# Kernel optimization log

Measured on AMD Instinct MI355X. Metric: run time of the kernel, lower is better.

The kernel has to match this reference:

```python
import jax, jax.numpy as jnp
import numpy as np

NEG_INF = -1e10  # matches torch's -10000000000.0 fill


def setup_inputs() -> dict:
    key = jax.random.key(0)
    k1, k2, k3, k4, k5, k6 = jax.random.split(key, 6)
    B, N, D_IN, D_HID, D_OUT = 8, 2048, 512, 512, 512
    H = jax.random.normal(k1, (B, N, D_IN), dtype=jnp.float32)
    bias = jax.random.normal(k2, (B, N, N), dtype=jnp.float32)
    mask = jax.random.randint(k3, (B, N, N), 0, 2, dtype=jnp.int32)
    s = 1.0 / np.sqrt(D_IN)
    Wq = jax.random.normal(k4, (D_IN, D_HID), dtype=jnp.float32) * s
    Wk = jax.random.normal(k5, (D_IN, D_HID), dtype=jnp.float32) * s
    Wv = jax.random.normal(k6, (D_IN, D_OUT), dtype=jnp.float32) * s
    return {"H": H, "bias": bias, "mask": mask, "Wq": Wq, "Wk": Wk, "Wv": Wv}


def reference(H, bias, mask, Wq, Wk, Wv):
    # Q,K: [B,N,d_hid], V: [B,N,d_out]
    Q = H @ Wq
    K = H @ Wk
    V = H @ Wv
    d = Q.shape[-1]
    scale = 1.0 / jnp.sqrt(jnp.asarray(d, dtype=Q.dtype))
    # scores: [B,N,N]; scale, add bias, then fill masked-out entries
    scores = jnp.einsum("bnd,bmd->bnm", Q, K) * scale + bias
    scores = jnp.where(mask == 0, jnp.asarray(NEG_INF, scores.dtype), scores)
    atn = jax.nn.softmax(scores, axis=-1)
    return jnp.einsum("bnm,bmo->bno", atn, V)
```

## Files before the change

### kernel.cpp

```cpp
#include <hip/hip_runtime.h>
#include <hip/hip_bf16.h>

typedef __attribute__((ext_vector_type(8))) short short8;
typedef __attribute__((ext_vector_type(4))) float floatx4;
typedef __attribute__((ext_vector_type(4))) int intx4;
typedef __attribute__((ext_vector_type(4))) unsigned short ushortx4;

#define NB 8
#define NN 2048
#define DD 512

__device__ __forceinline__ unsigned short f2bf(float f) {
  union { float f; unsigned int u; } v; v.f = f;
  unsigned int u = v.u;
  return (unsigned short)((u + 0x7fffu + ((u >> 16) & 1u)) >> 16);
}
__device__ __forceinline__ float bf2f(unsigned short s) {
  union { unsigned int u; float f; } v; v.u = ((unsigned int)s) << 16;
  return v.f;
}

typedef __attribute__((address_space(3))) unsigned short lds_us;
typedef __attribute__((address_space(1))) const unsigned short glb_us;

__device__ __forceinline__ void ld_lds16(const unsigned short* g, unsigned short* l) {
  __builtin_amdgcn_global_load_lds((glb_us*)g, (lds_us*)l, 16, 0, 0);
}

__global__ __launch_bounds__(256) void mha_cvtH(const float* __restrict__ H,
                                                unsigned short* __restrict__ Hb, int n8) {
  int i = blockIdx.x * 256 + threadIdx.x;
  if (i >= n8) return;
  const float4* src = (const float4*)H;
  float4 a = src[2 * i], b = src[2 * i + 1];
  short8 o;
  o[0] = (short)f2bf(a.x); o[1] = (short)f2bf(a.y); o[2] = (short)f2bf(a.z); o[3] = (short)f2bf(a.w);
  o[4] = (short)f2bf(b.x); o[5] = (short)f2bf(b.y); o[6] = (short)f2bf(b.z); o[7] = (short)f2bf(b.w);
  *(short8*)(Hb + 8 * i) = o;
}

__global__ __launch_bounds__(256) void mha_prep(const floatx4* __restrict__ bias,
                                                const intx4* __restrict__ mask,
                                                ushortx4* __restrict__ bm) {
  int i = blockIdx.x * 256 + threadIdx.x;
  floatx4 bv = __builtin_nontemporal_load(&bias[i]);
  intx4 mv = __builtin_nontemporal_load(&mask[i]);
  const unsigned short NINF = 0xFF80;
  ushortx4 o;
  o.x = mv.x ? f2bf(bv.x) : NINF;
  o.y = mv.y ? f2bf(bv.y) : NINF;
  o.z = mv.z ? f2bf(bv.z) : NINF;
  o.w = mv.w ? f2bf(bv.w) : NINF;
  __builtin_nontemporal_store(o, &bm[i]);
}

__global__ __launch_bounds__(256) void mha_tW(const float* __restrict__ Wq, const float* __restrict__ Wk,
                                              const float* __restrict__ Wv,
                                              unsigned short* __restrict__ Wqt, unsigned short* __restrict__ Wkt,
                                              unsigned short* __restrict__ Wvt) {
  const float* W = (blockIdx.z == 0) ? Wq : (blockIdx.z == 1) ? Wk : Wv;
  unsigned short* Wt = (blockIdx.z == 0) ? Wqt : (blockIdx.z == 1) ? Wkt : Wvt;
  __shared__ float tile[32][33];
  int d0 = blockIdx.x * 32, k0 = blockIdx.y * 32;
  int t = threadIdx.x, r = t >> 3, c4 = (t & 7) * 4;
  float4 v = *(const float4*)(W + (size_t)(k0 + r) * DD + d0 + c4);
  tile[r][c4] = v.x; tile[r][c4 + 1] = v.y; tile[r][c4 + 2] = v.z; tile[r][c4 + 3] = v.w;
  __syncthreads();
  union { unsigned short s[4]; uint2 v; } u;
  u.s[0] = f2bf(tile[c4][r]);     u.s[1] = f2bf(tile[c4 + 1][r]);
  u.s[2] = f2bf(tile[c4 + 2][r]); u.s[3] = f2bf(tile[c4 + 3][r]);
  *(uint2*)(Wt + (size_t)(d0 + r) * DD + k0 + c4) = u.v;
}

__global__ __launch_bounds__(256) void mha_tV(const unsigned short* __restrict__ Vr,
                                              unsigned short* __restrict__ Vt) {
  int b = blockIdx.z;
  int d0 = blockIdx.x * 32, n0 = blockIdx.y * 32;
  __shared__ unsigned short tile[32][34];
  int t = threadIdx.x, r = t >> 3, c4 = (t & 7) * 4;
  union { uint2 v; unsigned short s[4]; } u;
  u.v = *(const uint2*)(Vr + ((size_t)b * NN + n0 + r) * DD + d0 + c4);
  tile[r][c4] = u.s[0]; tile[r][c4 + 1] = u.s[1]; tile[r][c4 + 2] = u.s[2]; tile[r][c4 + 3] = u.s[3];
  __syncthreads();
  union { unsigned short s[4]; uint2 v; } o;
  o.s[0] = tile[c4][r]; o.s[1] = tile[c4 + 1][r]; o.s[2] = tile[c4 + 2][r]; o.s[3] = tile[c4 + 3][r];
  *(uint2*)(Vt + ((size_t)b * DD + d0 + r) * NN + n0 + c4) = o.v;
}

__device__ __forceinline__ void stage_tile_async(const unsigned short* __restrict__ g, int ld,
                                                 unsigned short* s, int t) {
#pragma unroll
  for (int h = 0; h < 2; ++h) {
    int c = t + h * 256;
    int r = c >> 2, p = c & 3;
    int seg = (p - (r >> 1)) & 3;
    ld_lds16(g + (size_t)r * ld + seg * 8, s + c * 8);
  }
}

__device__ __forceinline__ void mfma_step(const unsigned short* As, const unsigned short* Bs,
                                          int wr, int wc, int quad, int lr, floatx4 acc[4][4]) {
  short8 a[4], b[4];
#pragma unroll
  for (int i = 0; i < 4; ++i) {
    int ra = wr * 64 + i * 16 + lr;
    int rb = wc * 64 + i * 16 + lr;
    a[i] = *(const short8*)(As + ra * 32 + ((quad + (ra >> 1)) & 3) * 8);
    b[i] = *(const short8*)(Bs + rb * 32 + ((quad + (rb >> 1)) & 3) * 8);
  }
  __builtin_amdgcn_s_setprio(1);
#pragma unroll
  for (int i = 0; i < 4; ++i)
#pragma unroll
    for (int j = 0; j < 4; ++j)
      acc[i][j] = __builtin_amdgcn_mfma_f32_16x16x32_bf16(a[i], b[j], acc[i][j], 0, 0, 0);
  __builtin_amdgcn_s_setprio(0);
}

__global__ __launch_bounds__(256) void mha_proj(const unsigned short* __restrict__ Hb,
                                                const unsigned short* __restrict__ Wqt,
                                                const unsigned short* __restrict__ Wkt,
                                                const unsigned short* __restrict__ Wvt,
                                                unsigned short* __restrict__ Qb,
                                                unsigned short* __restrict__ Kb,
                                                unsigned short* __restrict__ Vr) {
  const unsigned short* Wt = (blockIdx.z == 0) ? Wqt : (blockIdx.z == 1) ? Wkt : Wvt;
  unsigned short* dst = (blockIdx.z == 0) ? Qb : (blockIdx.z == 1) ? Kb : Vr;
  __shared__ unsigned short As[128 * 64], Bs[128 * 64];
  int t = threadIdx.x, wave = t >> 6, lane = t & 63, quad = lane >> 4, lr = lane & 15;
  int wr = wave >> 1, wc = wave & 1;
  int m0 = blockIdx.y * 128, n0 = blockIdx.x * 128;
  floatx4 acc[4][4] = {};
  for (int k0 = 0; k0 < DD; k0 += 64) {
    __syncthreads();
    stage_tile_async(Hb + (size_t)m0 * DD + k0, DD, As, t);
    stage_tile_async(Hb + (size_t)m0 * DD + k0 + 32, DD, As + 4096, t);
    stage_tile_async(Wt + (size_t)n0 * DD + k0, DD, Bs, t);
    stage_tile_async(Wt + (size_t)n0 * DD + k0 + 32, DD, Bs + 4096, t);
    __syncthreads();
    mfma_step(As, Bs, wr, wc, quad, lr, acc);
    mfma_step(As + 4096, Bs + 4096, wr, wc, quad, lr, acc);
  }
#pragma unroll
  for (int i = 0; i < 4; ++i)
#pragma unroll
    for (int j = 0; j < 4; ++j)
#pragma unroll
      for (int r = 0; r < 4; ++r) {
        int row = m0 + wr * 64 + i * 16 + quad * 4 + r;
        int col = n0 + wc * 64 + j * 16 + lr;
        dst[(size_t)row * DD + col] = f2bf(acc[i][j][r]);
      }
}


template <int SQ>
__device__ __forceinline__ void qk_stage(const unsigned short* Ks, const short8* q,
                                         int wj, int quad, int lr, floatx4 (&acc_s)[4]) {
  __builtin_amdgcn_s_setprio(1);
#pragma unroll
  for (int kc = 0; kc < 4; ++kc) {
#pragma unroll
    for (int jt = 0; jt < 4; ++jt) {
      int rb = wj * 64 + jt * 16 + lr;
      short8 bf = *(const short8*)(Ks + kc * 4096 + rb * 32 + ((quad + (rb >> 1)) & 3) * 8);
      acc_s[jt] = __builtin_amdgcn_mfma_f32_16x16x32_bf16(q[SQ * 4 + kc], bf, acc_s[jt], 0, 0, 0);
    }
  }
  __builtin_amdgcn_s_setprio(0);
}

template <int JC>
__device__ __forceinline__ void pv_stage(const unsigned short* Vs, const unsigned short* Ps,
                                         int wave, int quad, int lr, floatx4 (&acc_o)[4][4]) {
  short8 pa[4];
#pragma unroll
  for (int it = 0; it < 4; ++it)
    pa[it] = *(const short8*)(Ps + (it * 16 + lr) * 128 + ((JC * 32 + quad * 8) ^ ((lr & 7) << 3)));
  __builtin_amdgcn_s_setprio(1);
#pragma unroll
  for (int dt = 0; dt < 4; ++dt) {
    int rb = wave * 64 + dt * 16 + lr;
    short8 bf = *(const short8*)(Vs + rb * 32 + ((quad + (rb >> 1)) & 3) * 8);
#pragma unroll
    for (int it = 0; it < 4; ++it)
      acc_o[it][dt] = __builtin_amdgcn_mfma_f32_16x16x32_bf16(pa[it], bf, acc_o[it][dt], 0, 0, 0);
  }
  __builtin_amdgcn_s_setprio(0);
}

__global__ __launch_bounds__(512) void mha_attn(const unsigned short* __restrict__ Qb,
                                                const unsigned short* __restrict__ Kb,
                                                const unsigned short* __restrict__ Vtb,
                                                const unsigned short* __restrict__ bmE,
                                                float* __restrict__ out) {
  __shared__ unsigned short KV[2][16384];
  __shared__ unsigned short Ps[64 * 128];
  __shared__ unsigned short Bm[64 * 128];
  __shared__ float ls[64];

  const int b = blockIdx.x;
  const int i0 = blockIdx.y * 64;
  const int t = threadIdx.x;
  const int wave = t >> 6, lane = t & 63, quad = lane >> 4, lr = lane & 15;
  const int wi = wave & 3;
  const int wj = wave >> 2;
  const float scale = 0.04419417382415922f;

  const unsigned short* Q = Qb + (size_t)b * NN * DD;
  const unsigned short* K = Kb + (size_t)b * NN * DD;
  const unsigned short* V = Vtb + (size_t)b * DD * NN;
  const unsigned short* bm = bmE + (size_t)b * NN * NN;

  if (t < 64) ls[t] = 0.0f;

  short8 q[16];
#pragma unroll
  for (int kc = 0; kc < 16; ++kc)
    q[kc] = *(const short8*)(Q + (size_t)(i0 + wi * 16 + lr) * DD + kc * 32 + quad * 8);

  floatx4 acc_o[4][4] = {};
  float rs[4] = {0.f, 0.f, 0.f, 0.f};

  const int krow = t >> 2, kphys = t & 3;
  const int kseg = (kphys - (krow >> 1)) & 3;

#pragma unroll
  for (int h = 0; h < 4; ++h)
    ld_lds16(K + (size_t)krow * DD + h * 32 + kseg * 8, KV[0] + h * 4096 + t * 8);
#pragma unroll
  for (int h = 0; h < 2; ++h) {
    int c = t + h * 512, row = c >> 4, phys = c & 15, seg = (phys - row) & 15;
    ld_lds16(bm + (size_t)(i0 + row) * NN + seg * 8, Bm + c * 8);
  }
  __syncthreads();

  for (int tt = 0; tt < 16; ++tt) {
    const int j0 = tt * 128;
    floatx4 acc_s[4] = {};

#pragma unroll
    for (int s = 0; s < 4; ++s) {
      if (s < 3) {
#pragma unroll
        for (int h = 0; h < 4; ++h)
          ld_lds16(K + (size_t)(j0 + krow) * DD + (s + 1) * 128 + h * 32 + kseg * 8,
                   KV[(s + 1) & 1] + h * 4096 + t * 8);
      } else {
#pragma unroll
        for (int h = 0; h < 4; ++h) {
          int c = t + h * 512, row = c >> 2, phys = c & 3, seg = (phys - (row >> 1)) & 3;
          ld_lds16(V + (size_t)row * NN + j0 + seg * 8, KV[0] + c * 8);
        }
      }
      if (s == 0) qk_stage<0>(KV[0], q, wj, quad, lr, acc_s);
      if (s == 1) qk_stage<1>(KV[1], q, wj, quad, lr, acc_s);
      if (s == 2) qk_stage<2>(KV[0], q, wj, quad, lr, acc_s);
      if (s == 3) {
        qk_stage<3>(KV[1], q, wj, quad, lr, acc_s);
#pragma unroll
        for (int jt = 0; jt < 4; ++jt) {
          int col = wj * 64 + jt * 16 + lr;
#pragma unroll
          for (int rr = 0; rr < 4; ++rr) {
            int row = wi * 16 + quad * 4 + rr;
            float bi = bf2f(Bm[row * 128 + ((((col >> 3) + row) & 15) << 3) + (col & 7)]);
            float e = __expf(acc_s[jt][rr] * scale + bi - 16.0f);
            unsigned short eb = f2bf(e);
            rs[rr] += bf2f(eb);
            Ps[row * 128 + (col ^ ((row & 7) << 3))] = eb;
          }
        }
      }
      __syncthreads();
    }

#pragma unroll
    for (int jc = 0; jc < 4; ++jc) {
      if (jc < 3) {
#pragma unroll
        for (int h = 0; h < 4; ++h) {
          int c = t + h * 512, row = c >> 2, phys = c & 3, seg = (phys - (row >> 1)) & 3;
          ld_lds16(V + (size_t)row * NN + j0 + (jc + 1) * 32 + seg * 8, KV[(jc + 1) & 1] + c * 8);
        }
      } else if (tt < 15) {
#pragma unroll
        for (int h = 0; h < 4; ++h)
          ld_lds16(K + (size_t)(j0 + 128 + krow) * DD + h * 32 + kseg * 8,
                   KV[0] + h * 4096 + t * 8);
#pragma unroll
        for (int h = 0; h < 2; ++h) {
          int c = t + h * 512, row = c >> 4, phys = c & 15, seg = (phys - row) & 15;
          ld_lds16(bm + (size_t)(i0 + row) * NN + j0 + 128 + seg * 8, Bm + c * 8);
        }
      }
      if (jc == 0) pv_stage<0>(KV[0], Ps, wave, quad, lr, acc_o);
      if (jc == 1) pv_stage<1>(KV[1], Ps, wave, quad, lr, acc_o);
      if (jc == 2) pv_stage<2>(KV[0], Ps, wave, quad, lr, acc_o);
      if (jc == 3) pv_stage<3>(KV[1], Ps, wave, quad, lr, acc_o);
      __syncthreads();
    }
  }

#pragma unroll
  for (int rr = 0; rr < 4; ++rr) {
    float v = rs[rr];
    v += __shfl_xor(v, 1);
    v += __shfl_xor(v, 2);
    v += __shfl_xor(v, 4);
    v += __shfl_xor(v, 8);
    if (lr == 0) atomicAdd(&ls[wi * 16 + quad * 4 + rr], v);
  }
  __syncthreads();

  float* ob = out + ((size_t)b * NN + i0) * DD;
#pragma unroll
  for (int it = 0; it < 4; ++it)
#pragma unroll
    for (int rr = 0; rr < 4; ++rr) {
      int row = it * 16 + quad * 4 + rr;
      float linv = 1.0f / ls[row];
#pragma unroll
      for (int dt = 0; dt < 4; ++dt)
        __builtin_nontemporal_store(acc_o[it][dt][rr] * linv,
                                    &ob[(size_t)row * DD + wave * 64 + dt * 16 + lr]);
    }
}

extern "C" void kernel_launch(void* const* d_in, const int* in_sizes, int n_in,
                              void* d_out, int out_size, void* d_ws, size_t ws_size,
                              hipStream_t stream) {
  const float* H = (const float*)d_in[0];
  const float* bias = (const float*)d_in[1];
  const int* mask = (const int*)d_in[2];
  const float* Wq = (const float*)d_in[3];
  const float* Wk = (const float*)d_in[4];
  const float* Wv = (const float*)d_in[5];
  float* out = (float*)d_out;
  char* ws = (char*)d_ws;

  const size_t SZ_QKV = (size_t)NB * NN * DD * 2;
  const size_t SZ_W = (size_t)DD * DD * 2;
  unsigned short* Qb = (unsigned short*)(ws);
  unsigned short* Kb = (unsigned short*)(ws + SZ_QKV);
  unsigned short* Vt = (unsigned short*)(ws + 2 * SZ_QKV);
  char* base2 = ws + 3 * SZ_QKV;
  unsigned short* bmE = (unsigned short*)(base2);
  unsigned short* Hb = (unsigned short*)(base2);
  unsigned short* Wqt = (unsigned short*)(base2 + SZ_QKV);
  unsigned short* Wkt = (unsigned short*)(base2 + SZ_QKV + SZ_W);
  unsigned short* Wvt = (unsigned short*)(base2 + SZ_QKV + 2 * SZ_W);
  unsigned short* Vr = (unsigned short*)(base2 + SZ_QKV + 3 * SZ_W);

  mha_cvtH<<<dim3((NB * NN * DD / 8) / 256), 256, 0, stream>>>(H, Hb, NB * NN * DD / 8);
  mha_tW<<<dim3(DD / 32, DD / 32, 3), 256, 0, stream>>>(Wq, Wk, Wv, Wqt, Wkt, Wvt);
  mha_proj<<<dim3(DD / 128, NB * NN / 128, 3), 256, 0, stream>>>(Hb, Wqt, Wkt, Wvt, Qb, Kb, Vr);
  mha_tV<<<dim3(DD / 32, NN / 32, NB), 256, 0, stream>>>(Vr, Vt);
  mha_prep<<<dim3((NB * NN * NN / 4) / 256), 256, 0, stream>>>((const floatx4*)bias,
                                                               (const intx4*)mask, (ushortx4*)bmE);
  mha_attn<<<dim3(NB, NN / 64), 512, 0, stream>>>(Qb, Kb, Vt, bmE, out);
}
```

Before: 489.8 us.

## Fuse bias/mask staging into attention and write V transposed from projection

Removes the separate bias+mask preprocessing pass, which read the fp32 bias and int32 mask and wrote a bf16 combined tensor. The attention kernel now streams raw fp32 bias and int32 mask tiles into LDS and applies the mask in the softmax step. The V projection epilogue writes its output already transposed, so the separate transpose kernel is dropped. The setprio hints around the MFMA blocks are also removed. LDS use grows substantially with the fp32 bias and int32 mask buffers, which may cut occupancy, and the attention loop now has to hide twice the global bytes for bias and mask.

New measurement: 536.8 us. 9.6% more time.

```diff
diff --git a/kernel.cpp b/kernel.cpp
--- a/kernel.cpp
+++ b/kernel.cpp
@@ -3,8 +3,6 @@
 
 typedef __attribute__((ext_vector_type(8))) short short8;
 typedef __attribute__((ext_vector_type(4))) float floatx4;
-typedef __attribute__((ext_vector_type(4))) int intx4;
-typedef __attribute__((ext_vector_type(4))) unsigned short ushortx4;
 
 #define NB 8
 #define NN 2048
@@ -37,21 +35,6 @@
   o[0] = (short)f2bf(a.x); o[1] = (short)f2bf(a.y); o[2] = (short)f2bf(a.z); o[3] = (short)f2bf(a.w);
   o[4] = (short)f2bf(b.x); o[5] = (short)f2bf(b.y); o[6] = (short)f2bf(b.z); o[7] = (short)f2bf(b.w);
   *(short8*)(Hb + 8 * i) = o;
-}
-
-__global__ __launch_bounds__(256) void mha_prep(const floatx4* __restrict__ bias,
-                                                const intx4* __restrict__ mask,
-                                                ushortx4* __restrict__ bm) {
-  int i = blockIdx.x * 256 + threadIdx.x;
-  floatx4 bv = __builtin_nontemporal_load(&bias[i]);
-  intx4 mv = __builtin_nontemporal_load(&mask[i]);
-  const unsigned short NINF = 0xFF80;
-  ushortx4 o;
-  o.x = mv.x ? f2bf(bv.x) : NINF;
-  o.y = mv.y ? f2bf(bv.y) : NINF;
-  o.z = mv.z ? f2bf(bv.z) : NINF;
-  o.w = mv.w ? f2bf(bv.w) : NINF;
-  __builtin_nontemporal_store(o, &bm[i]);
 }
 
 __global__ __launch_bounds__(256) void mha_tW(const float* __restrict__ Wq, const float* __restrict__ Wk,
@@ -72,21 +55,6 @@
   *(uint2*)(Wt + (size_t)(d0 + r) * DD + k0 + c4) = u.v;
 }
 
-__global__ __launch_bounds__(256) void mha_tV(const unsigned short* __restrict__ Vr,
-                                              unsigned short* __restrict__ Vt) {
-  int b = blockIdx.z;
-  int d0 = blockIdx.x * 32, n0 = blockIdx.y * 32;
-  __shared__ unsigned short tile[32][34];
-  int t = threadIdx.x, r = t >> 3, c4 = (t & 7) * 4;
-  union { uint2 v; unsigned short s[4]; } u;
-  u.v = *(const uint2*)(Vr + ((size_t)b * NN + n0 + r) * DD + d0 + c4);
-  tile[r][c4] = u.s[0]; tile[r][c4 + 1] = u.s[1]; tile[r][c4 + 2] = u.s[2]; tile[r][c4 + 3] = u.s[3];
-  __syncthreads();
-  union { unsigned short s[4]; uint2 v; } o;
-  o.s[0] = tile[c4][r]; o.s[1] = tile[c4 + 1][r]; o.s[2] = tile[c4 + 2][r]; o.s[3] = tile[c4 + 3][r];
-  *(uint2*)(Vt + ((size_t)b * DD + d0 + r) * NN + n0 + c4) = o.v;
-}
-
 __device__ __forceinline__ void stage_tile_async(const unsigned short* __restrict__ g, int ld,
                                                  unsigned short* s, int t) {
 #pragma unroll
@@ -108,13 +76,11 @@
     a[i] = *(const short8*)(As + ra * 32 + ((quad + (ra >> 1)) & 3) * 8);
     b[i] = *(const short8*)(Bs + rb * 32 + ((quad + (rb >> 1)) & 3) * 8);
   }
-  __builtin_amdgcn_s_setprio(1);
 #pragma unroll
   for (int i = 0; i < 4; ++i)
 #pragma unroll
     for (int j = 0; j < 4; ++j)
       acc[i][j] = __builtin_amdgcn_mfma_f32_16x16x32_bf16(a[i], b[j], acc[i][j], 0, 0, 0);
-  __builtin_amdgcn_s_setprio(0);
 }
 
 __global__ __launch_bounds__(256) void mha_proj(const unsigned short* __restrict__ Hb,
@@ -123,9 +89,8 @@
                                                 const unsigned short* __restrict__ Wvt,
                                                 unsigned short* __restrict__ Qb,
                                                 unsigned short* __restrict__ Kb,
-                                                unsigned short* __restrict__ Vr) {
+                                                unsigned short* __restrict__ Vt) {
   const unsigned short* Wt = (blockIdx.z == 0) ? Wqt : (blockIdx.z == 1) ? Wkt : Wvt;
-  unsigned short* dst = (blockIdx.z == 0) ? Qb : (blockIdx.z == 1) ? Kb : Vr;
   __shared__ unsigned short As[128 * 64], Bs[128 * 64];
   int t = threadIdx.x, wave = t >> 6, lane = t & 63, quad = lane >> 4, lr = lane & 15;
   int wr = wave >> 1, wc = wave & 1;
@@ -141,23 +106,39 @@
     mfma_step(As, Bs, wr, wc, quad, lr, acc);
     mfma_step(As + 4096, Bs + 4096, wr, wc, quad, lr, acc);
   }
-#pragma unroll
-  for (int i = 0; i < 4; ++i)
-#pragma unroll
-    for (int j = 0; j < 4; ++j)
-#pragma unroll
-      for (int r = 0; r < 4; ++r) {
-        int row = m0 + wr * 64 + i * 16 + quad * 4 + r;
+  if (blockIdx.z < 2) {
+    unsigned short* dst = (blockIdx.z == 0) ? Qb : Kb;
+#pragma unroll
+    for (int i = 0; i < 4; ++i)
+#pragma unroll
+      for (int j = 0; j < 4; ++j)
+#pragma unroll
+        for (int r = 0; r < 4; ++r) {
+          int row = m0 + wr * 64 + i * 16 + quad * 4 + r;
+          int col = n0 + wc * 64 + j * 16 + lr;
+          dst[(size_t)row * DD + col] = f2bf(acc[i][j][r]);
+        }
+  } else {
+    int bb = m0 >> 11;
+    int nbase = (m0 & (NN - 1)) + wr * 64 + quad * 4;
+#pragma unroll
+    for (int i = 0; i < 4; ++i)
+#pragma unroll
+      for (int j = 0; j < 4; ++j) {
         int col = n0 + wc * 64 + j * 16 + lr;
-        dst[(size_t)row * DD + col] = f2bf(acc[i][j][r]);
+        int nrow = nbase + i * 16;
+        union { unsigned short s[4]; uint2 v; } u;
+#pragma unroll
+        for (int r = 0; r < 4; ++r) u.s[r] = f2bf(acc[i][j][r]);
+        *(uint2*)(Vt + ((size_t)bb * DD + col) * NN + nrow) = u.v;
       }
+  }
 }
 
 
 template <int SQ>
 __device__ __forceinline__ void qk_stage(const unsigned short* Ks, const short8* q,
                                          int wj, int quad, int lr, floatx4 (&acc_s)[4]) {
-  __builtin_amdgcn_s_setprio(1);
 #pragma unroll
   for (int kc = 0; kc < 4; ++kc) {
 #pragma unroll
@@ -167,7 +148,6 @@
       acc_s[jt] = __builtin_amdgcn_mfma_f32_16x16x32_bf16(q[SQ * 4 + kc], bf, acc_s[jt], 0, 0, 0);
     }
   }
-  __builtin_amdgcn_s_setprio(0);
 }
 
 template <int JC>
@@ -177,7 +157,6 @@
 #pragma unroll
   for (int it = 0; it < 4; ++it)
     pa[it] = *(const short8*)(Ps + (it * 16 + lr) * 128 + ((JC * 32 + quad * 8) ^ ((lr & 7) << 3)));
-  __builtin_amdgcn_s_setprio(1);
 #pragma unroll
   for (int dt = 0; dt < 4; ++dt) {
     int rb = wave * 64 + dt * 16 + lr;
@@ -186,17 +165,18 @@
     for (int it = 0; it < 4; ++it)
       acc_o[it][dt] = __builtin_amdgcn_mfma_f32_16x16x32_bf16(pa[it], bf, acc_o[it][dt], 0, 0, 0);
   }
-  __builtin_amdgcn_s_setprio(0);
 }
 
 __global__ __launch_bounds__(512) void mha_attn(const unsigned short* __restrict__ Qb,
                                                 const unsigned short* __restrict__ Kb,
                                                 const unsigned short* __restrict__ Vtb,
-                                                const unsigned short* __restrict__ bmE,
+                                                const float* __restrict__ bias,
+                                                const int* __restrict__ mask,
                                                 float* __restrict__ out) {
   __shared__ unsigned short KV[2][16384];
   __shared__ unsigned short Ps[64 * 128];
-  __shared__ unsigned short Bm[64 * 128];
+  __shared__ float Bf[64 * 128];
+  __shared__ int Mi[64 * 128];
   __shared__ float ls[64];
 
   const int b = blockIdx.x;
@@ -210,10 +190,12 @@
   const unsigned short* Q = Qb + (size_t)b * NN * DD;
   const unsigned short* K = Kb + (size_t)b * NN * DD;
   const unsigned short* V = Vtb + (size_t)b * DD * NN;
-  const unsigned short* bm = bmE + (size_t)b * NN * NN;
+  const float* bg = bias + (size_t)b * NN * NN;
+  const int* mg = mask + (size_t)b * NN * NN;
 
   if (t < 64) ls[t] = 0.0f;
 
+  const int bmrow = t >> 5, bmphys = t & 31;
   short8 q[16];
 #pragma unroll
   for (int kc = 0; kc < 16; ++kc)
@@ -225,14 +207,26 @@
   const int krow = t >> 2, kphys = t & 3;
   const int kseg = (kphys - (krow >> 1)) & 3;
 
+#define STAGE_BIAS(H, J0)                                                                  \
+  {                                                                                        \
+    int c = t + (H) * 512, row = c >> 5, phys = c & 31, seg = (phys - row) & 31;           \
+    ld_lds16((const unsigned short*)(bg + (size_t)(i0 + row) * NN + (J0) + seg * 4),       \
+             (unsigned short*)Bf + c * 8);                                                 \
+  }
+#define STAGE_MASK(H, J0)                                                                  \
+  {                                                                                        \
+    int c = t + (H) * 512, row = c >> 5, phys = c & 31, seg = (phys - row) & 31;           \
+    ld_lds16((const unsigned short*)(mg + (size_t)(i0 + row) * NN + (J0) + seg * 4),       \
+             (unsigned short*)Mi + c * 8);                                                 \
+  }
+
 #pragma unroll
   for (int h = 0; h < 4; ++h)
     ld_lds16(K + (size_t)krow * DD + h * 32 + kseg * 8, KV[0] + h * 4096 + t * 8);
 #pragma unroll
-  for (int h = 0; h < 2; ++h) {
-    int c = t + h * 512, row = c >> 4, phys = c & 15, seg = (phys - row) & 15;
-    ld_lds16(bm + (size_t)(i0 + row) * NN + seg * 8, Bm + c * 8);
-  }
+  for (int h = 0; h < 4; ++h) STAGE_BIAS(h, 0)
+#pragma unroll
+  for (int h = 0; h < 4; ++h) STAGE_MASK(h, 0)
   __syncthreads();
 
   for (int tt = 0; tt < 16; ++tt) {
@@ -264,8 +258,10 @@
 #pragma unroll
           for (int rr = 0; rr < 4; ++rr) {
             int row = wi * 16 + quad * 4 + rr;
-            float bi = bf2f(Bm[row * 128 + ((((col >> 3) + row) & 15) << 3) + (col & 7)]);
-            float e = __expf(acc_s[jt][rr] * scale + bi - 16.0f);
+            int ph = ((col >> 2) + row) & 31, le = col & 3;
+            float bi = Bf[row * 128 + ph * 4 + le];
+            int mv = Mi[row * 128 + ph * 4 + le];
+            float e = mv ? __expf(acc_s[jt][rr] * scale + bi - 16.0f) : 0.0f;
             unsigned short eb = f2bf(e);
             rs[rr] += bf2f(eb);
             Ps[row * 128 + (col ^ ((row & 7) << 3))] = eb;
@@ -275,6 +271,7 @@
       __syncthreads();
     }
 
+    const int j0n = j0 + 128;
 #pragma unroll
     for (int jc = 0; jc < 4; ++jc) {
       if (jc < 3) {
@@ -283,16 +280,17 @@
           int c = t + h * 512, row = c >> 2, phys = c & 3, seg = (phys - (row >> 1)) & 3;
           ld_lds16(V + (size_t)row * NN + j0 + (jc + 1) * 32 + seg * 8, KV[(jc + 1) & 1] + c * 8);
         }
+        if (tt < 15) {
+          if (jc == 0) { STAGE_BIAS(0, j0n) STAGE_BIAS(1, j0n) }
+          if (jc == 1) { STAGE_BIAS(2, j0n) STAGE_BIAS(3, j0n) }
+          if (jc == 2) { STAGE_MASK(0, j0n) STAGE_MASK(1, j0n) }
+        }
       } else if (tt < 15) {
 #pragma unroll
         for (int h = 0; h < 4; ++h)
-          ld_lds16(K + (size_t)(j0 + 128 + krow) * DD + h * 32 + kseg * 8,
+          ld_lds16(K + (size_t)(j0n + krow) * DD + h * 32 + kseg * 8,
                    KV[0] + h * 4096 + t * 8);
-#pragma unroll
-        for (int h = 0; h < 2; ++h) {
-          int c = t + h * 512, row = c >> 4, phys = c & 15, seg = (phys - row) & 15;
-          ld_lds16(bm + (size_t)(i0 + row) * NN + j0 + 128 + seg * 8, Bm + c * 8);
-        }
+        STAGE_MASK(2, j0n) STAGE_MASK(3, j0n)
       }
       if (jc == 0) pv_stage<0>(KV[0], Ps, wave, quad, lr, acc_o);
       if (jc == 1) pv_stage<1>(KV[1], Ps, wave, quad, lr, acc_o);
@@ -345,18 +343,13 @@
   unsigned short* Kb = (unsigned short*)(ws + SZ_QKV);
   unsigned short* Vt = (unsigned short*)(ws + 2 * SZ_QKV);
   char* base2 = ws + 3 * SZ_QKV;
-  unsigned short* bmE = (unsigned short*)(base2);
   unsigned short* Hb = (unsigned short*)(base2);
   unsigned short* Wqt = (unsigned short*)(base2 + SZ_QKV);
   unsigned short* Wkt = (unsigned short*)(base2 + SZ_QKV + SZ_W);
   unsigned short* Wvt = (unsigned short*)(base2 + SZ_QKV + 2 * SZ_W);
-  unsigned short* Vr = (unsigned short*)(base2 + SZ_QKV + 3 * SZ_W);
 
   mha_cvtH<<<dim3((NB * NN * DD / 8) / 256), 256, 0, stream>>>(H, Hb, NB * NN * DD / 8);
   mha_tW<<<dim3(DD / 32, DD / 32, 3), 256, 0, stream>>>(Wq, Wk, Wv, Wqt, Wkt, Wvt);
-  mha_proj<<<dim3(DD / 128, NB * NN / 128, 3), 256, 0, stream>>>(Hb, Wqt, Wkt, Wvt, Qb, Kb, Vr);
-  mha_tV<<<dim3(DD / 32, NN / 32, NB), 256, 0, stream>>>(Vr, Vt);
-  mha_prep<<<dim3((NB * NN * NN / 4) / 256), 256, 0, stream>>>((const floatx4*)bias,
-                                                               (const intx4*)mask, (ushortx4*)bmE);
-  mha_attn<<<dim3(NB, NN / 64), 512, 0, stream>>>(Qb, Kb, Vt, bmE, out);
-}
+  mha_proj<<<dim3(DD / 128, NB * NN / 128, 3), 256, 0, stream>>>(Hb, Wqt, Wkt, Wvt, Qb, Kb, Vt);
+  mha_attn<<<dim3(NB, NN / 64), 512, 0, stream>>>(Qb, Kb, Vt, bias, mask, out);
+}
```
